# Kernel optimization log

Measured on AMD Instinct MI355X. Metric: run time of the kernel, lower is better.

Reference implementation:

```python
import jax, jax.numpy as jnp
import numpy as np

B = 8
N_GENES = 19836
D_IN = 11
D_H = 64
DEG = 16
N = B * N_GENES
E_PER = N_GENES * DEG


def setup_inputs() -> dict:
    key = jax.random.key(0)
    ks = jax.random.split(key, 20)
    x = jax.random.normal(ks[0], (B, N_GENES, D_IN), dtype=jnp.float32)
    # edges: random within each graph, offset by graph index
    base_src = jax.random.randint(ks[1], (B, E_PER), 0, N_GENES)
    base_dst = jax.random.randint(ks[2], (B, E_PER), 0, N_GENES)
    offs = (jnp.arange(B) * N_GENES)[:, None]
    src = (base_src + offs).reshape(-1).astype(jnp.int64) if False else (base_src + offs).reshape(-1)
    dst = (base_dst + offs).reshape(-1)
    s = 0.02
    def nrm(k, shape):
        return jax.random.normal(k, shape, dtype=jnp.float32) * s
    return {
        'x': x, 'src': src, 'dst': dst,
        'enc_W': nrm(ks[3], (D_H, D_IN)), 'enc_b': jnp.zeros((D_H,), jnp.float32),
        'gene_emb': nrm(ks[4], (N_GENES, D_H)),
        'gin_W': nrm(ks[5], (D_H, D_H)),
        'bn_w': 1.0 + nrm(ks[6], (D_H,)), 'bn_b': jnp.zeros((D_H,), jnp.float32),
        'key_W': nrm(ks[7], (D_H, D_H)), 'key_b': jnp.zeros((D_H,), jnp.float32),
        'query_w': nrm(ks[8], (1, D_H)),
        'val_W': nrm(ks[9], (D_H, D_H)), 'val_b': jnp.zeros((D_H,), jnp.float32),
        'sae_enc_W': nrm(ks[10], (D_H, D_H)), 'sae_enc_b': jnp.zeros((D_H,), jnp.float32),
        'sae_dec_W': nrm(ks[11], (D_H, D_H)), 'sae_dec_b': jnp.zeros((D_H,), jnp.float32),
        'pred_W1': nrm(ks[12], (D_H, D_H)), 'pred_b1': jnp.zeros((D_H,), jnp.float32),
        'pred_W2': nrm(ks[13], (1, D_H)), 'pred_b2': jnp.zeros((1,), jnp.float32),
    }


def gelu(x):
    return jax.nn.gelu(x, approximate=False)  # nn.GELU default = exact erf


def batchnorm(h, w, b, eps=1e-5):
    # training-mode BatchNorm1d: batch statistics, biased variance
    mu = jnp.mean(h, axis=0)
    var = jnp.mean((h - mu) ** 2, axis=0)
    return (h - mu) * jax.lax.rsqrt(var + eps) * w + b


def reference(x, src, dst, enc_W, enc_b, gene_emb, gin_W, bn_w, bn_b,
              key_W, key_b, query_w, val_W, val_b,
              sae_enc_W, sae_enc_b, sae_dec_W, sae_dec_b,
              pred_W1, pred_b1, pred_W2, pred_b2):
    bsz, n_gene, d_in = x.shape
    n_nodes = bsz * n_gene
    # gene encoder: single Linear (bias) + GELU (inner batchnorm result is discarded in source)
    h = gelu(x.reshape(-1, d_in) @ enc_W.T + enc_b)          # [N, D_H]
    h = (h.reshape(bsz, n_gene, -1) + gene_emb).reshape(n_nodes, -1)
    # GIN layer (eps=0, sum aggregation): MLP(h + sum_{u->v} h_u); MLP = single Linear, no bias
    agg = jax.ops.segment_sum(h[src], dst, num_segments=n_nodes)  # irregular gather/scatter
    h = (h + agg) @ gin_W.T
    h = gelu(batchnorm(h, bn_w, bn_b))
    # attentive readout with SAE
    keys = h @ key_W.T + key_b
    w = jax.nn.sigmoid(keys @ query_w.T)                     # [N, 1]
    v = h @ val_W.T + val_b
    z = v * w
    enc = jax.nn.relu(z @ sae_enc_W.T + sae_enc_b)
    dec = enc @ sae_dec_W.T + sae_dec_b
    sae_loss = jnp.mean((dec - z) ** 2) + 1.0 * jnp.mean(jnp.abs(enc))
    gid = jnp.arange(n_nodes) // n_gene
    g_h = jax.ops.segment_sum(dec * w, gid, num_segments=bsz)  # [B, D_H]
    # predictor: Linear+GELU, Linear (inner batchnorm discarded in source)
    preds = gelu(g_h @ pred_W1.T + pred_b1) @ pred_W2.T + pred_b2
    return preds, w, sae_loss, dec
```

## Files before the change

### kernel.cpp

```cpp
#include <hip/hip_runtime.h>
#include <math.h>

#define NGENES 19836
#define BATCH 8
#define DIN 11
#define DH 64
#define NNODES (BATCH * NGENES)
#define NEDGES (NNODES * 16)
#define NDH (NNODES * DH)
#define NGRP (NNODES / 4)

#define SCAN_CHUNK 1024
#define NSBLK ((NNODES + SCAN_CHUNK - 1) / SCAN_CHUNK)

#define OUT_PREDS 0
#define OUT_W 8
#define OUT_SAE (8 + NNODES)
#define OUT_DEC (9 + NNODES)

__device__ __forceinline__ float gelu_f(float x) {
    return 0.5f * x * (1.0f + erff(x * 0.70710678118654752f));
}

__device__ __forceinline__ float bcast(float v, int lane) {
    return __int_as_float(__builtin_amdgcn_readlane(__float_as_int(v), lane));
}

__device__ __forceinline__ float wave_sum(float v) {
    #pragma unroll
    for (int o = 32; o; o >>= 1) v += __shfl_xor(v, o, 64);
    return v;
}

__global__ void k_encoder(const float* __restrict__ x, const float* __restrict__ encW,
                          const float* __restrict__ encB, const float* __restrict__ gemb,
                          float* __restrict__ h) {
    int lane = threadIdx.x & 63;
    int wid = (blockIdx.x * blockDim.x + threadIdx.x) >> 6;
    int tw = (gridDim.x * blockDim.x) >> 6;
    int chunk = (NNODES + tw - 1) / tw;
    int start = wid * chunk;
    int end = min(start + chunk, NNODES);
    float wreg[DIN];
    #pragma unroll
    for (int k = 0; k < DIN; ++k) wreg[k] = encW[lane * DIN + k];
    float bias = encB[lane];
    for (int node = start; node < end; ++node) {
        const float* xr = x + (size_t)node * DIN;
        float acc = bias;
        #pragma unroll
        for (int k = 0; k < DIN; ++k) acc = fmaf(xr[k], wreg[k], acc);
        int gene = node % NGENES;
        h[(size_t)node * DH + lane] = gelu_f(acc) + gemb[(size_t)gene * DH + lane];
    }
}

__global__ void k_hist(const int* __restrict__ dst, int* __restrict__ counts) {
    int i = blockIdx.x * blockDim.x + threadIdx.x;
    int stride = gridDim.x * blockDim.x;
    for (int e = i; e < NEDGES; e += stride)
        atomicAdd(&counts[dst[e]], 1);
}

__global__ void k_scan1(const int* __restrict__ counts, int* __restrict__ bsum) {
    __shared__ int red[256];
    int base = blockIdx.x * SCAN_CHUNK + threadIdx.x * 4;
    int s = 0;
    #pragma unroll
    for (int i = 0; i < 4; ++i) {
        int n = base + i;
        if (n < NNODES) s += counts[n];
    }
    red[threadIdx.x] = s;
    __syncthreads();
    for (int o = 128; o; o >>= 1) {
        if (threadIdx.x < o) red[threadIdx.x] += red[threadIdx.x + o];
        __syncthreads();
    }
    if (threadIdx.x == 0) bsum[blockIdx.x] = red[0];
}

__global__ void k_scan2(const int* __restrict__ bsum, int* __restrict__ boff) {
    __shared__ int red[256];
    int t = threadIdx.x;
    int v = (t < NSBLK) ? bsum[t] : 0;
    red[t] = v;
    __syncthreads();
    for (int o = 1; o < 256; o <<= 1) {
        int u = (t >= o) ? red[t - o] : 0;
        __syncthreads();
        red[t] += u;
        __syncthreads();
    }
    if (t < NSBLK) boff[t] = red[t] - v;
}

__global__ void k_scan3(const int* __restrict__ counts, const int* __restrict__ boff,
                        int* __restrict__ offsets, int* __restrict__ cursor) {
    __shared__ int red[256];
    int t = threadIdx.x;
    int base = blockIdx.x * SCAN_CHUNK + t * 4;
    int c[4];
    int s = 0;
    #pragma unroll
    for (int i = 0; i < 4; ++i) {
        int n = base + i;
        c[i] = (n < NNODES) ? counts[n] : 0;
        s += c[i];
    }
    red[t] = s;
    __syncthreads();
    for (int o = 1; o < 256; o <<= 1) {
        int v = (t >= o) ? red[t - o] : 0;
        __syncthreads();
        red[t] += v;
        __syncthreads();
    }
    int excl = red[t] - s + boff[blockIdx.x];
    #pragma unroll
    for (int i = 0; i < 4; ++i) {
        int n = base + i;
        if (n < NNODES) { offsets[n] = excl; cursor[n] = excl; }
        excl += c[i];
    }
}

__global__ void k_scatter(const int* __restrict__ src, const int* __restrict__ dst,
                          int* __restrict__ cursor, unsigned short* __restrict__ csr) {
    int i = blockIdx.x * blockDim.x + threadIdx.x;
    int stride = gridDim.x * blockDim.x;
    for (int e = i; e < NEDGES; e += stride) {
        int p = atomicAdd(&cursor[dst[e]], 1);
        csr[p] = (unsigned short)(src[e] % NGENES);
    }
}

__global__ void __launch_bounds__(256, 3)
k_aggin(const float* __restrict__ h, const int* __restrict__ offsets,
        const int* __restrict__ counts, const unsigned short* __restrict__ csr,
        const float* __restrict__ ginW, float* __restrict__ h2,
        float* __restrict__ stats) {
    int lane = threadIdx.x & 63;
    int wid = (blockIdx.x * blockDim.x + threadIdx.x) >> 6;
    int tw = (gridDim.x * blockDim.x) >> 6;
    float wr[DH];
    #pragma unroll
    for (int k = 0; k < DH; ++k) wr[k] = ginW[lane * DH + k];
    float s1 = 0.f, s2 = 0.f;
    for (int node = wid; node < NNODES; node += tw) {
        int gbase = (node / NGENES) * NGENES;
        float a[8];
        a[0] = h[(size_t)node * DH + lane];
        #pragma unroll
        for (int i = 1; i < 8; ++i) a[i] = 0.f;
        int start = offsets[node];
        int cnt = counts[node];
        for (int e0 = 0; e0 < cnt; e0 += 64) {
            int nn = min(64, cnt - e0);
            int iv = (lane < nn) ? (int)csr[start + e0 + lane] : 0;
            int j = 0;
            for (; j + 7 < nn; j += 8) {
                #pragma unroll
                for (int u = 0; u < 8; ++u) {
                    int v = gbase + __shfl(iv, j + u, 64);
                    a[u] += h[(size_t)v * DH + lane];
                }
            }
            for (; j < nn; ++j)
                a[0] += h[(size_t)(gbase + __shfl(iv, j, 64)) * DH + lane];
        }
        float tval = ((a[0] + a[1]) + (a[2] + a[3])) + ((a[4] + a[5]) + (a[6] + a[7]));
        float m0 = 0.f, m1 = 0.f, m2 = 0.f, m3 = 0.f;
        #pragma unroll
        for (int k = 0; k < DH; k += 4) {
            m0 = fmaf(wr[k], bcast(tval, k), m0);
            m1 = fmaf(wr[k + 1], bcast(tval, k + 1), m1);
            m2 = fmaf(wr[k + 2], bcast(tval, k + 2), m2);
            m3 = fmaf(wr[k + 3], bcast(tval, k + 3), m3);
        }
        float outv = (m0 + m1) + (m2 + m3);
        h2[(size_t)node * DH + lane] = outv;
        s1 += outv;
        s2 += outv * outv;
    }
    __shared__ float red[2][256];
    red[0][threadIdx.x] = s1;
    red[1][threadIdx.x] = s2;
    __syncthreads();
    if (threadIdx.x < 64) {
        float t1 = red[0][threadIdx.x] + red[0][threadIdx.x + 64] + red[0][threadIdx.x + 128] + red[0][threadIdx.x + 192];
        float t2 = red[1][threadIdx.x] + red[1][threadIdx.x + 64] + red[1][threadIdx.x + 128] + red[1][threadIdx.x + 192];
        atomicAdd(&stats[threadIdx.x], t1);
        atomicAdd(&stats[64 + threadIdx.x], t2);
    }
}

__global__ void k_bnparams(const float* __restrict__ stats, const float* __restrict__ bnw,
                           const float* __restrict__ bnb, const float* __restrict__ keyW,
                           const float* __restrict__ keyB, const float* __restrict__ qw,
                           float* __restrict__ bnp) {
    int d = threadIdx.x;
    float inv_n = 1.0f / (float)NNODES;
    float mu = stats[d] * inv_n;
    float var = stats[64 + d] * inv_n - mu * mu;
    float sc = bnw[d] * rsqrtf(var + 1e-5f);
    bnp[d] = sc;
    bnp[64 + d] = bnb[d] - mu * sc;
    float kq0 = 0.f, kq1 = 0.f;
    #pragma unroll
    for (int j = 0; j < DH; j += 2) {
        kq0 = fmaf(qw[j], keyW[j * DH + d], kq0);
        kq1 = fmaf(qw[j + 1], keyW[(j + 1) * DH + d], kq1);
    }
    bnp[128 + d] = kq0 + kq1;
    float qb = wave_sum(qw[d] * keyB[d]);
    if (d == 0) bnp[192] = qb;
}

__global__ void __launch_bounds__(256, 3)
k_attn(float* __restrict__ h2, const float* __restrict__ bnp,
       const float* __restrict__ valW, const float* __restrict__ valB,
       float* __restrict__ wout) {
    int lane = threadIdx.x & 63;
    int wid = (blockIdx.x * blockDim.x + threadIdx.x) >> 6;
    int tw = (gridDim.x * blockDim.x) >> 6;
    int chunk = (NGRP + tw - 1) / tw;
    int gs = wid * chunk;
    int ge = min(gs + chunk, NGRP);
    float vw[DH];
    #pragma unroll
    for (int k = 0; k < DH; ++k) vw[k] = valW[lane * DH + k];
    float vb = valB[lane], sc = bnp[lane], sh = bnp[64 + lane], kq = bnp[128 + lane];
    float qb = bnp[192];
    for (int g = gs; g < ge; ++g) {
        int node = g * 4;
        float h3[4], p[4];
        #pragma unroll
        for (int i = 0; i < 4; ++i) {
            float hv = h2[(size_t)(node + i) * DH + lane];
            h3[i] = gelu_f(fmaf(hv, sc, sh));
            p[i] = h3[i] * kq;
        }
        #pragma unroll
        for (int o = 32; o; o >>= 1) {
            #pragma unroll
            for (int i = 0; i < 4; ++i) p[i] += __shfl_xor(p[i], o, 64);
        }
        float wq[4];
        #pragma unroll
        for (int i = 0; i < 4; ++i) wq[i] = 1.0f / (1.0f + expf(-(p[i] + qb)));
        float a[4];
        #pragma unroll
        for (int i = 0; i < 4; ++i) a[i] = 0.f;
        #pragma unroll
        for (int k = 0; k < DH; ++k) {
            #pragma unroll
            for (int i = 0; i < 4; ++i) a[i] = fmaf(vw[k], bcast(h3[i], k), a[i]);
        }
        #pragma unroll
        for (int i = 0; i < 4; ++i)
            h2[(size_t)(node + i) * DH + lane] = (a[i] + vb) * wq[i];
        if (lane == 0) {
            wout[node] = wq[0]; wout[node + 1] = wq[1];
            wout[node + 2] = wq[2]; wout[node + 3] = wq[3];
        }
    }
}

__global__ void __launch_bounds__(256, 2)
k_sae(const float* __restrict__ zbuf, const float* __restrict__ encW,
      const float* __restrict__ encB, const float* __restrict__ decW,
      const float* __restrict__ decB, const float* __restrict__ wout,
      float* __restrict__ decout, float* __restrict__ g_h,
      float* __restrict__ loss) {
    int lane = threadIdx.x & 63;
    int wid = (blockIdx.x * blockDim.x + threadIdx.x) >> 6;
    int tw = (gridDim.x * blockDim.x) >> 6;
    int chunk = (NGRP + tw - 1) / tw;
    int gs = wid * chunk;
    int ge = min(gs + chunk, NGRP);
    float ew[DH], dw[DH];
    #pragma unroll
    for (int k = 0; k < DH; ++k) {
        ew[k] = encW[lane * DH + k];
        dw[k] = decW[lane * DH + k];
    }
    float eb = encB[lane], db = decB[lane];
    float sq = 0.f, l1 = 0.f, gacc = 0.f;
    int cur_g = (gs < NGRP) ? (gs * 4) / NGENES : 0;
    for (int g = gs; g < ge; ++g) {
        int node = g * 4;
        int gg = node / NGENES;
        if (gg != cur_g) {
            atomicAdd(&g_h[cur_g * DH + lane], gacc);
            gacc = 0.f;
            cur_g = gg;
        }
        float z[4], e[4], enc[4], d[4];
        #pragma unroll
        for (int i = 0; i < 4; ++i) {
            z[i] = zbuf[(size_t)(node + i) * DH + lane];
            e[i] = 0.f;
        }
        #pragma unroll
        for (int k = 0; k < DH; ++k) {
            #pragma unroll
            for (int i = 0; i < 4; ++i) e[i] = fmaf(ew[k], bcast(z[i], k), e[i]);
        }
        #pragma unroll
        for (int i = 0; i < 4; ++i) {
            enc[i] = fmaxf(e[i] + eb, 0.0f);
            d[i] = 0.f;
        }
        #pragma unroll
        for (int k = 0; k < DH; ++k) {
            #pragma unroll
            for (int i = 0; i < 4; ++i) d[i] = fmaf(dw[k], bcast(enc[i], k), d[i]);
        }
        #pragma unroll
        for (int i = 0; i < 4; ++i) {
            float dec = d[i] + db;
            float wq = wout[node + i];
            decout[(size_t)(node + i) * DH + lane] = dec;
            float diff = dec - z[i];
            sq = fmaf(diff, diff, sq);
            l1 += fabsf(enc[i]);
            gacc = fmaf(dec, wq, gacc);
        }
    }
    if (gs < ge) atomicAdd(&g_h[cur_g * DH + lane], gacc);
    sq = wave_sum(sq);
    l1 = wave_sum(l1);
    if (lane == 0) {
        atomicAdd(&loss[0], sq);
        atomicAdd(&loss[1], l1);
    }
}

__global__ void k_pred(const float* __restrict__ g_h, const float* __restrict__ W1,
                       const float* __restrict__ b1, const float* __restrict__ W2,
                       const float* __restrict__ b2, const float* __restrict__ loss,
                       float* __restrict__ out) {
    int lane = threadIdx.x;
    float w1[DH];
    #pragma unroll
    for (int k = 0; k < DH; ++k) w1[k] = W1[lane * DH + k];
    float bb = b1[lane], w2 = W2[lane];
    for (int g = 0; g < BATCH; ++g) {
        float gh = g_h[g * DH + lane];
        float a0 = 0.f, a1 = 0.f;
        #pragma unroll
        for (int k = 0; k < DH; k += 2) {
            a0 = fmaf(w1[k], bcast(gh, k), a0);
            a1 = fmaf(w1[k + 1], bcast(gh, k + 1), a1);
        }
        float t = gelu_f(a0 + a1 + bb);
        float p = wave_sum(t * w2);
        if (lane == 0) out[OUT_PREDS + g] = p + b2[0];
    }
    if (lane == 0) out[OUT_SAE] = (loss[0] + loss[1]) * (1.0f / ((float)NNODES * (float)DH));
}

extern "C" void kernel_launch(void* const* d_in, const int* in_sizes, int n_in,
                              void* d_out, int out_size, void* d_ws, size_t ws_size,
                              hipStream_t stream) {
    const float* x    = (const float*)d_in[0];
    const int* src    = (const int*)d_in[1];
    const int* dst    = (const int*)d_in[2];
    const float* encW = (const float*)d_in[3];
    const float* encB = (const float*)d_in[4];
    const float* gemb = (const float*)d_in[5];
    const float* ginW = (const float*)d_in[6];
    const float* bnw  = (const float*)d_in[7];
    const float* bnb  = (const float*)d_in[8];
    const float* keyW = (const float*)d_in[9];
    const float* keyB = (const float*)d_in[10];
    const float* qw   = (const float*)d_in[11];
    const float* valW = (const float*)d_in[12];
    const float* valB = (const float*)d_in[13];
    const float* saeEncW = (const float*)d_in[14];
    const float* saeEncB = (const float*)d_in[15];
    const float* saeDecW = (const float*)d_in[16];
    const float* saeDecB = (const float*)d_in[17];
    const float* pW1  = (const float*)d_in[18];
    const float* pb1  = (const float*)d_in[19];
    const float* pW2  = (const float*)d_in[20];
    const float* pb2  = (const float*)d_in[21];

    float* out = (float*)d_out;
    float* ws = (float*)d_ws;

    int*   counts  = (int*)ws;
    float* stats   = ws + NNODES;
    float* g_h     = stats + 128;
    float* loss    = g_h + 512;
    float* bnp     = loss + 2;
    int*   offsets = (int*)(bnp + 256);
    int*   cursor  = offsets + NNODES;
    unsigned short* csr = (unsigned short*)(cursor + NNODES);
    int*   bsum    = (int*)(csr + NEDGES);
    int*   boff    = bsum + 256;
    float* h2      = (float*)(boff + 256);

    float* h    = out + OUT_DEC;
    float* wout = out + OUT_W;

    hipMemsetAsync(d_ws, 0, (size_t)(NNODES + 642) * sizeof(float), stream);

    k_encoder<<<2048, 256, 0, stream>>>(x, encW, encB, gemb, h);
    k_hist<<<2048, 256, 0, stream>>>(dst, counts);
    k_scan1<<<NSBLK, 256, 0, stream>>>(counts, bsum);
    k_scan2<<<1, 256, 0, stream>>>(bsum, boff);
    k_scan3<<<NSBLK, 256, 0, stream>>>(counts, boff, offsets, cursor);
    k_scatter<<<2048, 256, 0, stream>>>(src, dst, cursor, csr);
    k_aggin<<<2048, 256, 0, stream>>>(h, offsets, counts, csr, ginW, h2, stats);
    k_bnparams<<<1, 64, 0, stream>>>(stats, bnw, bnb, keyW, keyB, qw, bnp);
    k_attn<<<2048, 256, 0, stream>>>(h2, bnp, valW, valB, wout);
    k_sae<<<2048, 256, 0, stream>>>(h2, saeEncW, saeEncB, saeDecW, saeDecB, wout, h, g_h, loss);
    k_pred<<<1, 64, 0, stream>>>(g_h, pW1, pb1, pW2, pb2, loss, out);
}
```

Before: 898.9 us.

## Map one node per lane in attention and SAE kernels, split graph readout

The attention and SAE kernels now assign one node per lane, hold the 64-wide node vector in registers, and read the weight matrices as wave-uniform scalar loads. This replaces the per-feature-lane layout that needed cross-lane readlane broadcasts and shuffle reductions. Each lane now reads and writes a 256-byte row with float4 accesses, which is strided across the wave rather than coalesced. The per-graph weighted sum of dec moves into a separate k_ghsum kernel, adding one launch and a reread of dec.

Measured after the change: 1.077 ms. +19.8%, slower.

```diff
diff --git a/kernel.cpp b/kernel.cpp
--- a/kernel.cpp
+++ b/kernel.cpp
@@ -8,7 +8,7 @@
 #define NNODES (BATCH * NGENES)
 #define NEDGES (NNODES * 16)
 #define NDH (NNODES * DH)
-#define NGRP (NNODES / 4)
+#define NWAVE ((NNODES + 63) / 64)
 
 #define SCAN_CHUNK 1024
 #define NSBLK ((NNODES + SCAN_CHUNK - 1) / SCAN_CHUNK)
@@ -222,119 +222,128 @@
        const float* __restrict__ valW, const float* __restrict__ valB,
        float* __restrict__ wout) {
     int lane = threadIdx.x & 63;
-    int wid = (blockIdx.x * blockDim.x + threadIdx.x) >> 6;
-    int tw = (gridDim.x * blockDim.x) >> 6;
-    int chunk = (NGRP + tw - 1) / tw;
-    int gs = wid * chunk;
-    int ge = min(gs + chunk, NGRP);
-    float vw[DH];
-    #pragma unroll
-    for (int k = 0; k < DH; ++k) vw[k] = valW[lane * DH + k];
-    float vb = valB[lane], sc = bnp[lane], sh = bnp[64 + lane], kq = bnp[128 + lane];
-    float qb = bnp[192];
-    for (int g = gs; g < ge; ++g) {
-        int node = g * 4;
-        float h3[4], p[4];
-        #pragma unroll
-        for (int i = 0; i < 4; ++i) {
-            float hv = h2[(size_t)(node + i) * DH + lane];
-            h3[i] = gelu_f(fmaf(hv, sc, sh));
-            p[i] = h3[i] * kq;
-        }
-        #pragma unroll
-        for (int o = 32; o; o >>= 1) {
+    int wv = (blockIdx.x * blockDim.x + threadIdx.x) >> 6;
+    int node = wv * 64 + lane;
+    bool act = node < NNODES;
+    float* row = h2 + (size_t)node * DH;
+    float h3[DH];
+    if (act) {
+        #pragma unroll
+        for (int j = 0; j < 16; ++j) {
+            float4 v = *reinterpret_cast<const float4*>(row + j * 4);
+            h3[j * 4] = v.x; h3[j * 4 + 1] = v.y; h3[j * 4 + 2] = v.z; h3[j * 4 + 3] = v.w;
+        }
+    } else {
+        #pragma unroll
+        for (int k = 0; k < DH; ++k) h3[k] = 0.f;
+    }
+    float p = bnp[192];
+    #pragma unroll
+    for (int k = 0; k < DH; ++k) {
+        h3[k] = gelu_f(fmaf(h3[k], bnp[k], bnp[64 + k]));
+        p = fmaf(h3[k], bnp[128 + k], p);
+    }
+    float wq = 1.0f / (1.0f + expf(-p));
+    if (act) wout[node] = wq;
+    #pragma unroll
+    for (int d4 = 0; d4 < DH; d4 += 4) {
+        float a[4];
+        #pragma unroll
+        for (int j = 0; j < 4; ++j) {
+            float acc = valB[d4 + j];
             #pragma unroll
-            for (int i = 0; i < 4; ++i) p[i] += __shfl_xor(p[i], o, 64);
-        }
-        float wq[4];
-        #pragma unroll
-        for (int i = 0; i < 4; ++i) wq[i] = 1.0f / (1.0f + expf(-(p[i] + qb)));
-        float a[4];
-        #pragma unroll
-        for (int i = 0; i < 4; ++i) a[i] = 0.f;
-        #pragma unroll
-        for (int k = 0; k < DH; ++k) {
-            #pragma unroll
-            for (int i = 0; i < 4; ++i) a[i] = fmaf(vw[k], bcast(h3[i], k), a[i]);
-        }
-        #pragma unroll
-        for (int i = 0; i < 4; ++i)
-            h2[(size_t)(node + i) * DH + lane] = (a[i] + vb) * wq[i];
-        if (lane == 0) {
-            wout[node] = wq[0]; wout[node + 1] = wq[1];
-            wout[node + 2] = wq[2]; wout[node + 3] = wq[3];
-        }
-    }
-}
-
-__global__ void __launch_bounds__(256, 2)
+            for (int k = 0; k < DH; ++k)
+                acc = fmaf(valW[(d4 + j) * DH + k], h3[k], acc);
+            a[j] = acc * wq;
+        }
+        if (act) {
+            float4 v = { a[0], a[1], a[2], a[3] };
+            *reinterpret_cast<float4*>(row + d4) = v;
+        }
+    }
+}
+
+__global__ void __launch_bounds__(256, 3)
 k_sae(const float* __restrict__ zbuf, const float* __restrict__ encW,
       const float* __restrict__ encB, const float* __restrict__ decW,
-      const float* __restrict__ decB, const float* __restrict__ wout,
-      float* __restrict__ decout, float* __restrict__ g_h,
+      const float* __restrict__ decB, float* __restrict__ decout,
       float* __restrict__ loss) {
     int lane = threadIdx.x & 63;
-    int wid = (blockIdx.x * blockDim.x + threadIdx.x) >> 6;
-    int tw = (gridDim.x * blockDim.x) >> 6;
-    int chunk = (NGRP + tw - 1) / tw;
-    int gs = wid * chunk;
-    int ge = min(gs + chunk, NGRP);
-    float ew[DH], dw[DH];
-    #pragma unroll
-    for (int k = 0; k < DH; ++k) {
-        ew[k] = encW[lane * DH + k];
-        dw[k] = decW[lane * DH + k];
-    }
-    float eb = encB[lane], db = decB[lane];
-    float sq = 0.f, l1 = 0.f, gacc = 0.f;
-    int cur_g = (gs < NGRP) ? (gs * 4) / NGENES : 0;
-    for (int g = gs; g < ge; ++g) {
-        int node = g * 4;
-        int gg = node / NGENES;
-        if (gg != cur_g) {
-            atomicAdd(&g_h[cur_g * DH + lane], gacc);
-            gacc = 0.f;
-            cur_g = gg;
-        }
-        float z[4], e[4], enc[4], d[4];
-        #pragma unroll
-        for (int i = 0; i < 4; ++i) {
-            z[i] = zbuf[(size_t)(node + i) * DH + lane];
-            e[i] = 0.f;
-        }
-        #pragma unroll
-        for (int k = 0; k < DH; ++k) {
+    int wv = (blockIdx.x * blockDim.x + threadIdx.x) >> 6;
+    int node = wv * 64 + lane;
+    bool act = node < NNODES;
+    const float* zr = zbuf + (size_t)node * DH;
+    float z[DH];
+    if (act) {
+        #pragma unroll
+        for (int j = 0; j < 16; ++j) {
+            float4 v = *reinterpret_cast<const float4*>(zr + j * 4);
+            z[j * 4] = v.x; z[j * 4 + 1] = v.y; z[j * 4 + 2] = v.z; z[j * 4 + 3] = v.w;
+        }
+    } else {
+        #pragma unroll
+        for (int k = 0; k < DH; ++k) z[k] = 0.f;
+    }
+    float enc[DH];
+    float l1 = 0.f;
+    #pragma unroll
+    for (int d = 0; d < DH; ++d) {
+        float a = encB[d];
+        #pragma unroll
+        for (int k = 0; k < DH; ++k) a = fmaf(encW[d * DH + k], z[k], a);
+        enc[d] = fmaxf(a, 0.f);
+        l1 += enc[d];
+    }
+    float sq = 0.f;
+    float* dr = decout + (size_t)node * DH;
+    #pragma unroll
+    for (int d4 = 0; d4 < DH; d4 += 4) {
+        float a[4];
+        #pragma unroll
+        for (int j = 0; j < 4; ++j) {
+            float acc = decB[d4 + j];
             #pragma unroll
-            for (int i = 0; i < 4; ++i) e[i] = fmaf(ew[k], bcast(z[i], k), e[i]);
-        }
-        #pragma unroll
-        for (int i = 0; i < 4; ++i) {
-            enc[i] = fmaxf(e[i] + eb, 0.0f);
-            d[i] = 0.f;
-        }
-        #pragma unroll
-        for (int k = 0; k < DH; ++k) {
-            #pragma unroll
-            for (int i = 0; i < 4; ++i) d[i] = fmaf(dw[k], bcast(enc[i], k), d[i]);
-        }
-        #pragma unroll
-        for (int i = 0; i < 4; ++i) {
-            float dec = d[i] + db;
-            float wq = wout[node + i];
-            decout[(size_t)(node + i) * DH + lane] = dec;
-            float diff = dec - z[i];
+            for (int k = 0; k < DH; ++k)
+                acc = fmaf(decW[(d4 + j) * DH + k], enc[k], acc);
+            a[j] = acc;
+            float diff = acc - z[d4 + j];
             sq = fmaf(diff, diff, sq);
-            l1 += fabsf(enc[i]);
-            gacc = fmaf(dec, wq, gacc);
-        }
-    }
-    if (gs < ge) atomicAdd(&g_h[cur_g * DH + lane], gacc);
+        }
+        if (act) {
+            float4 v = { a[0], a[1], a[2], a[3] };
+            *reinterpret_cast<float4*>(dr + d4) = v;
+        }
+    }
+    if (!act) { sq = 0.f; l1 = 0.f; }
     sq = wave_sum(sq);
     l1 = wave_sum(l1);
     if (lane == 0) {
         atomicAdd(&loss[0], sq);
         atomicAdd(&loss[1], l1);
     }
+}
+
+__global__ void k_ghsum(const float* __restrict__ dec, const float* __restrict__ wout,
+                        float* __restrict__ g_h) {
+    int lane = threadIdx.x & 63;
+    int wid = (blockIdx.x * blockDim.x + threadIdx.x) >> 6;
+    int tw = (gridDim.x * blockDim.x) >> 6;
+    int chunk = (NNODES + tw - 1) / tw;
+    int gs = wid * chunk;
+    int ge = min(gs + chunk, NNODES);
+    if (gs >= ge) return;
+    float gacc = 0.f;
+    int cur_g = gs / NGENES;
+    for (int n = gs; n < ge; ++n) {
+        int g = n / NGENES;
+        if (g != cur_g) {
+            atomicAdd(&g_h[cur_g * DH + lane], gacc);
+            gacc = 0.f;
+            cur_g = g;
+        }
+        gacc = fmaf(dec[(size_t)n * DH + lane], wout[n], gacc);
+    }
+    atomicAdd(&g_h[cur_g * DH + lane], gacc);
 }
 
 __global__ void k_pred(const float* __restrict__ g_h, const float* __restrict__ W1,
@@ -415,7 +424,8 @@
     k_scatter<<<2048, 256, 0, stream>>>(src, dst, cursor, csr);
     k_aggin<<<2048, 256, 0, stream>>>(h, offsets, counts, csr, ginW, h2, stats);
     k_bnparams<<<1, 64, 0, stream>>>(stats, bnw, bnb, keyW, keyB, qw, bnp);
-    k_attn<<<2048, 256, 0, stream>>>(h2, bnp, valW, valB, wout);
-    k_sae<<<2048, 256, 0, stream>>>(h2, saeEncW, saeEncB, saeDecW, saeDecB, wout, h, g_h, loss);
+    k_attn<<<(NWAVE + 3) / 4, 256, 0, stream>>>(h2, bnp, valW, valB, wout);
+    k_sae<<<(NWAVE + 3) / 4, 256, 0, stream>>>(h2, saeEncW, saeEncB, saeDecW, saeDecB, h, loss);
+    k_ghsum<<<512, 256, 0, stream>>>(h, wout, g_h);
     k_pred<<<1, 64, 0, stream>>>(g_h, pW1, pb1, pW2, pb2, loss, out);
 }
```
